# Kernel tuning notes

Measured on AMD Instinct MI355X. Metric: run time of the kernel, lower is better.

## Reference

```python
import jax, jax.numpy as jnp
import numpy as np

B, S, HID = 2, 2048, 2048
H, HKV, D = 8, 4, 256
SW = 1024
SOFTCAP = 50.0
SCALE = D ** -0.5
NEG = -2.3819763e38
ROPE_BASE = 10000.0


def _rope(x, cos, sin):
    # x: [B, S, H, D]; cos/sin: [S, D/2]. Gemma: first half real, second half imag.
    d2 = x.shape[-1] // 2
    x1, x2 = x[..., :d2], x[..., d2:]
    c = cos[None, :, None, :]
    s = sin[None, :, None, :]
    return jnp.concatenate([x1 * c - x2 * s, x1 * s + x2 * c], axis=-1)


def setup_inputs() -> dict:
    key = jax.random.key(0)
    k1, k2, k3, k4, k5, k6 = jax.random.split(key, 6)
    hidden_states = jax.random.normal(k1, (B, S, HID), dtype=jnp.float32)
    # Gemma RoPE freqs_cis -> cos/sin tables [S, D/2]
    inv_freq = 1.0 / (ROPE_BASE ** (np.arange(0, D, 2, dtype=np.float32) / D))
    t = np.arange(S, dtype=np.float32)
    ang = np.outer(t, inv_freq)  # [S, D/2]
    freqs_cos = jnp.asarray(np.cos(ang), dtype=jnp.float32)
    freqs_sin = jnp.asarray(np.sin(ang), dtype=jnp.float32)
    # causal additive mask [1,1,S,S]
    i = jnp.arange(S)
    causal = i[:, None] >= i[None, :]
    mask = jnp.where(causal, 0.0, NEG).astype(jnp.float32)[None, None]
    std = HID ** -0.5
    wq = jax.random.normal(k2, (H * D, HID), dtype=jnp.float32) * std
    wk = jax.random.normal(k3, (HKV * D, HID), dtype=jnp.float32) * std
    wv = jax.random.normal(k4, (HKV * D, HID), dtype=jnp.float32) * std
    wo = jax.random.normal(k5, (HID, H * D), dtype=jnp.float32) * (H * D) ** -0.5
    return {"hidden_states": hidden_states, "freqs_cos": freqs_cos,
            "freqs_sin": freqs_sin, "mask": mask,
            "wq": wq, "wk": wk, "wv": wv, "wo": wo}


def reference(hidden_states, freqs_cos, freqs_sin, mask, wq, wk, wv, wo):
    b, s, _ = hidden_states.shape
    q = (hidden_states @ wq.T).reshape(b, s, H, D)
    k = (hidden_states @ wk.T).reshape(b, s, HKV, D)
    v = (hidden_states @ wv.T).reshape(b, s, HKV, D)
    q = _rope(q, freqs_cos, freqs_sin)
    k = _rope(k, freqs_cos, freqs_sin)
    # GQA: repeat_interleave kv heads to match query heads
    rep = H // HKV
    k = jnp.repeat(k, rep, axis=2)
    v = jnp.repeat(v, rep, axis=2)
    q = q.transpose(0, 2, 1, 3)  # [B,H,S,D]
    k = k.transpose(0, 2, 1, 3)
    v = v.transpose(0, 2, 1, 3)
    # local (sliding window) mask: keep |i-j| <= SW-1, else NEG
    i = jnp.arange(s)
    rel = i[:, None] - i[None, :]
    sliding = jnp.abs(rel) < SW
    mask = jnp.where(sliding[None, None], mask, NEG)
    # scaled scores with tanh logit softcapping
    scores = jnp.einsum('bhqd,bhkd->bhqk', q * SCALE, k)
    scores = jnp.tanh(scores / SOFTCAP) * SOFTCAP
    scores = scores + mask
    probs = jax.nn.softmax(scores.astype(jnp.float32), axis=-1).astype(q.dtype)
    attn_output = jnp.einsum('bhqk,bhkd->bhqd', probs, v)  # [B,H,S,D]
    out = attn_output.transpose(0, 2, 1, 3).reshape(b, s, H * D) @ wo.T
    return out, probs, attn_output
```

## Files before the change

### kernel.cpp

```cpp
#include <hip/hip_runtime.h>
#include <hip/hip_bf16.h>

typedef __bf16 bfx8 __attribute__((ext_vector_type(8)));
typedef float  floatx4 __attribute__((ext_vector_type(4)));

#define B_   2
#define S_   2048
#define HID_ 2048
#define H_   8
#define HKV_ 4
#define D_   256
#define SW_  1024
#define NTOK (B_*S_)

__device__ __forceinline__ bool inputs_are_f32(const void* fc) {
  return *(const unsigned int*)fc == 0x3F800000u;
}

__device__ __forceinline__ bfx8 cvt8(const float* p) {
  floatx4 a = *(const floatx4*)p, b = *(const floatx4*)(p + 4);
  bfx8 r;
#pragma unroll
  for (int i = 0; i < 4; ++i) { r[i] = (__bf16)a[i]; r[i + 4] = (__bf16)b[i]; }
  return r;
}

__device__ __forceinline__ bfx8 ld8(const void* base, size_t eoff, bool f32m) {
  if (f32m) return cvt8((const float*)base + eoff);
  return *(const bfx8*)((const __bf16*)base + eoff);
}

__global__ __launch_bounds__(256)
void cvt_f32_bf16(const void* __restrict__ in, __bf16* __restrict__ out,
                  int n8, const void* __restrict__ fcp)
{
  const bool f32m = inputs_are_f32(fcp);
  int i = blockIdx.x * 256 + threadIdx.x;
  int stride = gridDim.x * 256;
  for (; i < n8; i += stride) {
    if (f32m) ((bfx8*)out)[i] = cvt8((const float*)in + (size_t)i * 8);
    else      ((bfx8*)out)[i] = ((const bfx8*)in)[i];
  }
}

template<int SWZ>
__device__ __forceinline__ void xcd_tile(int& bx, int& by) {
  int gx = gridDim.x;
  int orig = blockIdx.y * gx + blockIdx.x;
  int xcd = orig & 7, loc = orig >> 3;
  if (SWZ == 1) {
    int wpx = gx >> 3;
    if (wpx <= 1) { bx = xcd; by = loc; }
    else { bx = (xcd << 1) + (loc & 1); by = loc >> 1; }
  } else {
    int hpy = gridDim.y >> 3;
    int r = loc / gx;
    by = xcd * hpy + r;
    bx = loc - r * gx;
  }
}

template<int AMODE, int EPI, int DT, int SWZ>
__global__ __launch_bounds__(256)
void gemm_bt(const void* __restrict__ A, const void* __restrict__ Bm,
             void* __restrict__ C, const void* __restrict__ fcp,
             int K, int lda, int ldb, int ldc)
{
  const bool f32m = (DT == 1) ? false : inputs_are_f32(fcp);
  __shared__ __align__(16) __bf16 As[128*40];
  __shared__ __align__(16) __bf16 Bs[128*40];
  const int tid  = threadIdx.x;
  const int lane = tid & 63, wave = tid >> 6;
  int bx, by;
  xcd_tile<SWZ>(bx, by);
  const int m0 = by * 128, n0 = bx * 128;
  const int waveM = (wave >> 1) * 64, waveN = (wave & 1) * 64;
  const int lr = lane & 15, quad = lane >> 4;
  floatx4 acc[4][4] = {};

  for (int k0 = 0; k0 < K; k0 += 32) {
    __syncthreads();
#pragma unroll
    for (int cc = 0; cc < 2; ++cc) {
      int c = tid + cc * 256;
      int row = c >> 2, q = c & 3;
      bfx8 av;
      if (AMODE == 0) {
        av = ld8(A, (size_t)(m0 + row) * lda + (k0 + q * 8), f32m);
      } else {
        int mg = m0 + row, kk = k0 + q * 8;
        size_t aoff = ((size_t)((mg >> 11) * H_ + (kk >> 8)) * S_ + (mg & (S_ - 1))) * D_ + (kk & (D_ - 1));
        av = cvt8((const float*)A + aoff);
      }
      *(bfx8*)(&As[row * 40 + q * 8]) = av;
      *(bfx8*)(&Bs[row * 40 + q * 8]) = ld8(Bm, (size_t)(n0 + row) * ldb + (k0 + q * 8), f32m);
    }
    __syncthreads();
    bfx8 af[4], bfr[4];
#pragma unroll
    for (int im = 0; im < 4; ++im)
      af[im] = *(const bfx8*)(&As[(waveM + im * 16 + lr) * 40 + quad * 8]);
#pragma unroll
    for (int in = 0; in < 4; ++in)
      bfr[in] = *(const bfx8*)(&Bs[(waveN + in * 16 + lr) * 40 + quad * 8]);
#pragma unroll
    for (int im = 0; im < 4; ++im)
#pragma unroll
      for (int in = 0; in < 4; ++in)
        acc[im][in] = __builtin_amdgcn_mfma_f32_16x16x32_bf16(af[im], bfr[in], acc[im][in], 0, 0, 0);
  }

#pragma unroll
  for (int im = 0; im < 4; ++im)
#pragma unroll
    for (int in = 0; in < 4; ++in)
#pragma unroll
      for (int r = 0; r < 4; ++r) {
        int rg = m0 + waveM + im * 16 + quad * 4 + r;
        int cg = n0 + waveN + in * 16 + lr;
        float v = acc[im][in][r];
        if (EPI == 0) ((float*)C)[(size_t)rg * ldc + cg] = v;
        else          ((__bf16*)C)[(size_t)rg * ldc + cg] = (__bf16)v;
      }
}

__global__ __launch_bounds__(256)
void rope_kernel(float* __restrict__ qreg, float* __restrict__ kreg,
                 const void* __restrict__ fc, const void* __restrict__ fs)
{
  const bool f32m = inputs_are_f32(fc);
  int tok = blockIdx.x, t = threadIdx.x;
  int spos = tok & (S_ - 1);
  const float* qrow = qreg + (size_t)tok * 2048;
  const float* krow = kreg + (size_t)tok * 1024;
  float xq1[4], xq2[4], xk1[2], xk2[2];
#pragma unroll
  for (int p = 0; p < 4; ++p) {
    int idx = p * 256 + t, h = idx >> 7, d = idx & 127;
    xq1[p] = qrow[h * 256 + d]; xq2[p] = qrow[h * 256 + d + 128];
  }
#pragma unroll
  for (int p = 0; p < 2; ++p) {
    int idx = p * 256 + t, h = idx >> 7, d = idx & 127;
    xk1[p] = krow[h * 256 + d]; xk2[p] = krow[h * 256 + d + 128];
  }
  __syncthreads();
  __bf16* qo = (__bf16*)qreg + (size_t)tok * 4096;
  __bf16* ko = (__bf16*)kreg + (size_t)tok * 2048;
#pragma unroll
  for (int p = 0; p < 4; ++p) {
    int idx = p * 256 + t, h = idx >> 7, d = idx & 127;
    float c = f32m ? ((const float*)fc)[spos * 128 + d] : (float)((const __bf16*)fc)[spos * 128 + d];
    float s = f32m ? ((const float*)fs)[spos * 128 + d] : (float)((const __bf16*)fs)[spos * 128 + d];
    qo[h * 256 + d]       = (__bf16)((xq1[p] * c - xq2[p] * s) * 0.0625f);
    qo[h * 256 + d + 128] = (__bf16)((xq1[p] * s + xq2[p] * c) * 0.0625f);
  }
#pragma unroll
  for (int p = 0; p < 2; ++p) {
    int idx = p * 256 + t, h = idx >> 7, d = idx & 127;
    float c = f32m ? ((const float*)fc)[spos * 128 + d] : (float)((const __bf16*)fc)[spos * 128 + d];
    float s = f32m ? ((const float*)fs)[spos * 128 + d] : (float)((const __bf16*)fs)[spos * 128 + d];
    ko[h * 256 + d]       = (__bf16)(xk1[p] * c - xk2[p] * s);
    ko[h * 256 + d + 128] = (__bf16)(xk1[p] * s + xk2[p] * c);
  }
}

__global__ __launch_bounds__(256)
void qk_mfma(const __bf16* __restrict__ qr, const __bf16* __restrict__ kr,
             float* __restrict__ probs)
{
  const int bh = blockIdx.z;
  const int b = bh >> 3, h = bh & 7, hkv = h >> 1;
  const int i0 = blockIdx.y * 128;
  const int j0 = i0 - 1024 + blockIdx.x * 128;
  if (j0 + 128 <= 0) return;
  __shared__ __align__(16) __bf16 As[128*40];
  __shared__ __align__(16) __bf16 Bs[128*40];
  const int tid  = threadIdx.x;
  const int lane = tid & 63, wave = tid >> 6;
  const int waveM = (wave >> 1) * 64, waveN = (wave & 1) * 64;
  const int lr = lane & 15, quad = lane >> 4;
  floatx4 acc[4][4] = {};
  const __bf16* qbase = qr + ((size_t)(b * S_) << 12) + h * D_;
  const __bf16* kbase = kr + ((size_t)(b * S_) << 11) + hkv * D_;

  for (int k0 = 0; k0 < D_; k0 += 32) {
    __syncthreads();
#pragma unroll
    for (int cc = 0; cc < 2; ++cc) {
      int c = tid + cc * 256;
      int row = c >> 2, q = c & 3;
      int kk = k0 + q * 8;
      *(bfx8*)(&As[row * 40 + q * 8]) = *(const bfx8*)(qbase + ((size_t)(i0 + row) << 12) + kk);
      int jrow = j0 + row; int jc = jrow < 0 ? 0 : jrow;
      *(bfx8*)(&Bs[row * 40 + q * 8]) = *(const bfx8*)(kbase + ((size_t)jc << 11) + kk);
    }
    __syncthreads();
    bfx8 af[4], bfr[4];
#pragma unroll
    for (int im = 0; im < 4; ++im)
      af[im] = *(const bfx8*)(&As[(waveM + im * 16 + lr) * 40 + quad * 8]);
#pragma unroll
    for (int in = 0; in < 4; ++in)
      bfr[in] = *(const bfx8*)(&Bs[(waveN + in * 16 + lr) * 40 + quad * 8]);
#pragma unroll
    for (int im = 0; im < 4; ++im)
#pragma unroll
      for (int in = 0; in < 4; ++in)
        acc[im][in] = __builtin_amdgcn_mfma_f32_16x16x32_bf16(af[im], bfr[in], acc[im][in], 0, 0, 0);
  }

#pragma unroll
  for (int im = 0; im < 4; ++im)
#pragma unroll
    for (int in = 0; in < 4; ++in)
#pragma unroll
      for (int r = 0; r < 4; ++r) {
        int rg = i0 + waveM + im * 16 + quad * 4 + r;
        int cg = j0 + waveN + in * 16 + lr;
        if (cg >= 0) {
          float v = acc[im][in][r];
          float e = __expf(0.04f * v);
          probs[((size_t)bh * S_ + rg) * 2048 + cg] =
              50.f * (e - 1.f) * __builtin_amdgcn_rcpf(e + 1.f);
        }
      }
}

__global__ __launch_bounds__(256)
void softmax_nat(float* __restrict__ probs)
{
  int i = blockIdx.x, bh = blockIdx.y;
  float* row = probs + ((size_t)bh * S_ + i) * 2048;
  int t = threadIdx.x;
  int jlo = (i >= 1023) ? (i - 1023) : 0;
  __shared__ float red[256];

  float lm = -3.0e38f;
  for (int j = jlo + t; j <= i; j += 256) lm = fmaxf(lm, row[j]);
  red[t] = lm; __syncthreads();
  for (int st = 128; st; st >>= 1) { if (t < st) red[t] = fmaxf(red[t], red[t + st]); __syncthreads(); }
  float mx = red[0]; __syncthreads();

  float ls = 0.f;
  for (int j = jlo + t; j <= i; j += 256) ls += __expf(row[j] - mx);
  red[t] = ls; __syncthreads();
  for (int st = 128; st; st >>= 1) { if (t < st) red[t] += red[t + st]; __syncthreads(); }
  float inv = 1.f / red[0];

  float pv[8];
#pragma unroll
  for (int rep = 0; rep < 8; ++rep) {
    int j = t + rep * 256;
    bool valid = (j >= jlo) && (j <= i);
    pv[rep] = valid ? __expf(row[j] - mx) * inv : 0.f;
  }
  __syncthreads();
#pragma unroll
  for (int rep = 0; rep < 8; ++rep) row[t + rep * 256] = pv[rep];
}

__global__ __launch_bounds__(256)
void transpose_v(const __bf16* __restrict__ vb, __bf16* __restrict__ vt)
{
  __shared__ __align__(16) __bf16 tile[64 * 72];
  int b = blockIdx.z, c0 = blockIdx.y * 64, j0 = blockIdx.x * 64;
  int tid = threadIdx.x;
#pragma unroll
  for (int p = 0; p < 2; ++p) {
    int e = p * 2048 + tid * 8;
    int row = e >> 6, col = e & 63;
    int swz = col ^ (((row >> 3) & 7) * 8);
    *(bfx8*)(&tile[row * 72 + swz]) =
      *(const bfx8*)(vb + ((size_t)(b * S_ + j0 + row) << 10) + c0 + col);
  }
  __syncthreads();
#pragma unroll
  for (int p = 0; p < 2; ++p) {
    int e = p * 2048 + tid * 8;
    int cc = e >> 6, jj = e & 63;
    bfx8 v8;
#pragma unroll
    for (int x = 0; x < 8; ++x) {
      int row = jj + x;
      v8[x] = tile[row * 72 + (cc ^ (((row >> 3) & 7) * 8))];
    }
    *(bfx8*)(vt + ((size_t)(b * 1024 + c0 + cc) << 11) + j0 + jj) = v8;
  }
}

__global__ __launch_bounds__(256)
void pv_mfma(const float* __restrict__ probs, const __bf16* __restrict__ vt,
             float* __restrict__ attn)
{
  const int bh = blockIdx.z;
  const int b = bh >> 3, hkv = (bh & 7) >> 1;
  const int i0 = blockIdx.y * 128;
  const int n0 = blockIdx.x * 128;
  const int kstart = (i0 >= 1024) ? (i0 - 1024) : 0;
  const int kend = i0 + 128;
  __shared__ __align__(16) __bf16 As[128*40];
  __shared__ __align__(16) __bf16 Bs[128*40];
  const int tid  = threadIdx.x;
  const int lane = tid & 63, wave = tid >> 6;
  const int waveM = (wave >> 1) * 64, waveN = (wave & 1) * 64;
  const int lr = lane & 15, quad = lane >> 4;
  floatx4 acc[4][4] = {};
  const float*  abase = probs + ((size_t)bh * S_) * 2048;
  const __bf16* bbase = vt + ((size_t)(b * 1024 + hkv * 256 + n0)) * 2048;

  for (int k0 = kstart; k0 < kend; k0 += 32) {
    __syncthreads();
#pragma unroll
    for (int cc = 0; cc < 2; ++cc) {
      int c = tid + cc * 256;
      int row = c >> 2, q = c & 3;
      int kk = k0 + q * 8;
      *(bfx8*)(&As[row * 40 + q * 8]) = cvt8(abase + (size_t)(i0 + row) * 2048 + kk);
      *(bfx8*)(&Bs[row * 40 + q * 8]) = *(const bfx8*)(bbase + ((size_t)row << 11) + kk);
    }
    __syncthreads();
    bfx8 af[4], bfr[4];
#pragma unroll
    for (int im = 0; im < 4; ++im)
      af[im] = *(const bfx8*)(&As[(waveM + im * 16 + lr) * 40 + quad * 8]);
#pragma unroll
    for (int in = 0; in < 4; ++in)
      bfr[in] = *(const bfx8*)(&Bs[(waveN + in * 16 + lr) * 40 + quad * 8]);
#pragma unroll
    for (int im = 0; im < 4; ++im)
#pragma unroll
      for (int in = 0; in < 4; ++in)
        acc[im][in] = __builtin_amdgcn_mfma_f32_16x16x32_bf16(af[im], bfr[in], acc[im][in], 0, 0, 0);
  }

#pragma unroll
  for (int im = 0; im < 4; ++im)
#pragma unroll
    for (int in = 0; in < 4; ++in)
#pragma unroll
      for (int r = 0; r < 4; ++r) {
        int rg = i0 + waveM + im * 16 + quad * 4 + r;
        int cg = n0 + waveN + in * 16 + lr;
        attn[((size_t)bh * S_ + rg) * D_ + cg] = acc[im][in][r];
      }
}

extern "C" void kernel_launch(void* const* d_in, const int* in_sizes, int n_in,
                              void* d_out, int out_size, void* d_ws, size_t ws_size,
                              hipStream_t stream) {
  (void)in_sizes; (void)n_in; (void)out_size; (void)d_ws; (void)ws_size;
  const void* hidden = d_in[0];
  const void* fc     = d_in[1];
  const void* fs     = d_in[2];
  const void* wq     = d_in[4];
  const void* wk     = d_in[5];
  const void* wv     = d_in[6];
  const void* wo     = d_in[7];

  float* out_r   = (float*)d_out;
  float* probs_r = out_r + (size_t)B_ * S_ * HID_;
  float* attn_r  = probs_r + (size_t)B_ * H_ * S_ * S_;

  float*  qf = attn_r;
  __bf16* qr = (__bf16*)attn_r;
  float*  kf = out_r;
  __bf16* kr = (__bf16*)out_r;
  __bf16* vb = (__bf16*)out_r + 8388608;
  __bf16* vt = (__bf16*)(out_r + 6291456);

  __bf16* hb  = (__bf16*)probs_r;
  __bf16* wqb = hb  + (size_t)NTOK * HID_;
  __bf16* wkb = wqb + (size_t)H_ * D_ * HID_;
  __bf16* wvb = wkb + (size_t)HKV_ * D_ * HID_;

  dim3 blk(256);
  cvt_f32_bf16<<<dim3(1024), blk, 0, stream>>>(hidden, hb,  NTOK * HID_ / 8, fc);
  cvt_f32_bf16<<<dim3(512),  blk, 0, stream>>>(wq, wqb, H_ * D_ * HID_ / 8, fc);
  cvt_f32_bf16<<<dim3(256),  blk, 0, stream>>>(wk, wkb, HKV_ * D_ * HID_ / 8, fc);
  cvt_f32_bf16<<<dim3(256),  blk, 0, stream>>>(wv, wvb, HKV_ * D_ * HID_ / 8, fc);

  gemm_bt<0,0,1,1><<<dim3(16,32), blk, 0, stream>>>(hb, wqb, qf, fc, 2048, 2048, 2048, 2048);
  gemm_bt<0,0,1,1><<<dim3(8,32),  blk, 0, stream>>>(hb, wkb, kf, fc, 2048, 2048, 2048, 1024);
  gemm_bt<0,1,1,1><<<dim3(8,32),  blk, 0, stream>>>(hb, wvb, vb, fc, 2048, 2048, 2048, 1024);
  rope_kernel<<<dim3(NTOK), blk, 0, stream>>>(qf, kf, fc, fs);
  transpose_v<<<dim3(32,16,2), blk, 0, stream>>>(vb, vt);
  qk_mfma<<<dim3(9,16,16), blk, 0, stream>>>(qr, kr, probs_r);
  softmax_nat<<<dim3(2048,16), blk, 0, stream>>>(probs_r);
  pv_mfma<<<dim3(2,16,16), blk, 0, stream>>>(probs_r, vt, attn_r);
  gemm_bt<1,0,0,2><<<dim3(16,32), blk, 0, stream>>>(attn_r, wo, out_r, fc, 2048, 2048, 2048, 2048);
}
```

Baseline: 859.8 us.

## Fuse QK scores with softmax via two-pass recompute and widen PV tile

Replaces the separate QK score kernel and row softmax kernel with one kernel. It keeps a 64-row Q tile in LDS and runs over the sliding-window K tiles twice: the first pass builds row sums and the second recomputes scores and writes normalized probabilities. It uses a fixed exponent offset, which is safe because the tanh softcap bounds scores to ±50. The block also zero-fills the masked regions, so the full probs matrix is written once instead of written, read and rewritten. The PV kernel is widened to cover all 256 head columns per block, so each probs tile is loaded and converted once rather than twice. The cost is doubled QK MFMA work, lower occupancy from 64KB of LDS, and more accumulator registers in PV.

New measurement: 837.3 us. 2.6% less time.

```diff
diff --git a/kernel.cpp b/kernel.cpp
--- a/kernel.cpp
+++ b/kernel.cpp
@@ -166,98 +166,91 @@
 }
 
 __global__ __launch_bounds__(256)
-void qk_mfma(const __bf16* __restrict__ qr, const __bf16* __restrict__ kr,
-             float* __restrict__ probs)
-{
-  const int bh = blockIdx.z;
-  const int b = bh >> 3, h = bh & 7, hkv = h >> 1;
-  const int i0 = blockIdx.y * 128;
-  const int j0 = i0 - 1024 + blockIdx.x * 128;
-  if (j0 + 128 <= 0) return;
-  __shared__ __align__(16) __bf16 As[128*40];
-  __shared__ __align__(16) __bf16 Bs[128*40];
-  const int tid  = threadIdx.x;
-  const int lane = tid & 63, wave = tid >> 6;
-  const int waveM = (wave >> 1) * 64, waveN = (wave & 1) * 64;
+void qk_fused(const __bf16* __restrict__ qr, const __bf16* __restrict__ kr,
+              float* __restrict__ probs)
+{
+  const int bh = blockIdx.y, b = bh >> 3, h = bh & 7, hkv = h >> 1;
+  const int i0 = blockIdx.x * 64;
+  __shared__ __align__(16) __bf16 Qs[64*256];
+  __shared__ __align__(16) __bf16 Ks[64*256];
+  const int tid = threadIdx.x, lane = tid & 63, wave = tid >> 6;
   const int lr = lane & 15, quad = lane >> 4;
-  floatx4 acc[4][4] = {};
-  const __bf16* qbase = qr + ((size_t)(b * S_) << 12) + h * D_;
+  const int sx = lr & 7;
+  const __bf16* qbase = qr + ((size_t)(b * S_ + i0) << 12) + h * D_;
   const __bf16* kbase = kr + ((size_t)(b * S_) << 11) + hkv * D_;
 
-  for (int k0 = 0; k0 < D_; k0 += 32) {
-    __syncthreads();
-#pragma unroll
-    for (int cc = 0; cc < 2; ++cc) {
-      int c = tid + cc * 256;
-      int row = c >> 2, q = c & 3;
-      int kk = k0 + q * 8;
-      *(bfx8*)(&As[row * 40 + q * 8]) = *(const bfx8*)(qbase + ((size_t)(i0 + row) << 12) + kk);
-      int jrow = j0 + row; int jc = jrow < 0 ? 0 : jrow;
-      *(bfx8*)(&Bs[row * 40 + q * 8]) = *(const bfx8*)(kbase + ((size_t)jc << 11) + kk);
-    }
-    __syncthreads();
-    bfx8 af[4], bfr[4];
-#pragma unroll
-    for (int im = 0; im < 4; ++im)
-      af[im] = *(const bfx8*)(&As[(waveM + im * 16 + lr) * 40 + quad * 8]);
-#pragma unroll
-    for (int in = 0; in < 4; ++in)
-      bfr[in] = *(const bfx8*)(&Bs[(waveN + in * 16 + lr) * 40 + quad * 8]);
-#pragma unroll
-    for (int im = 0; im < 4; ++im)
+#pragma unroll
+  for (int p = 0; p < 8; ++p) {
+    int c = tid + p * 256;
+    int row = c >> 5, ch = c & 31;
+    *(bfx8*)(&Qs[row * 256 + (ch ^ (row & 7)) * 8]) =
+        *(const bfx8*)(qbase + ((size_t)row << 12) + ch * 8);
+  }
+
+  const int jt0 = (i0 >= 1024) ? 0 : (16 - (i0 >> 6));
+  const int myrow = wave * 16 + quad * 4;
+  float psum[4] = {0.f, 0.f, 0.f, 0.f};
+  float inv[4];
+
+  for (int pass = 0; pass < 2; ++pass) {
+    for (int jt = jt0; jt <= 16; ++jt) {
+      int j0 = i0 - 1024 + jt * 64;
+      __syncthreads();
+#pragma unroll
+      for (int p = 0; p < 8; ++p) {
+        int c = tid + p * 256;
+        int row = c >> 5, ch = c & 31;
+        *(bfx8*)(&Ks[row * 256 + (ch ^ (row & 7)) * 8]) =
+            *(const bfx8*)(kbase + ((size_t)(j0 + row) << 11) + ch * 8);
+      }
+      __syncthreads();
+      floatx4 acc[4] = {};
+#pragma unroll
+      for (int ks = 0; ks < 8; ++ks) {
+        bfx8 af = *(const bfx8*)(&Qs[(wave * 16 + lr) * 256 + ((ks * 4 + quad) ^ sx) * 8]);
+#pragma unroll
+        for (int in = 0; in < 4; ++in) {
+          bfx8 bf = *(const bfx8*)(&Ks[(in * 16 + lr) * 256 + ((ks * 4 + quad) ^ sx) * 8]);
+          acc[in] = __builtin_amdgcn_mfma_f32_16x16x32_bf16(af, bf, acc[in], 0, 0, 0);
+        }
+      }
 #pragma unroll
       for (int in = 0; in < 4; ++in)
-        acc[im][in] = __builtin_amdgcn_mfma_f32_16x16x32_bf16(af[im], bfr[in], acc[im][in], 0, 0, 0);
-  }
-
-#pragma unroll
-  for (int im = 0; im < 4; ++im)
-#pragma unroll
-    for (int in = 0; in < 4; ++in)
+#pragma unroll
+        for (int r = 0; r < 4; ++r) {
+          int rg = i0 + myrow + r;
+          int cg = j0 + in * 16 + lr;
+          bool valid = (cg <= rg) && (rg - cg < SW_);
+          float v = acc[in][r];
+          float e = __expf(0.04f * v);
+          float sc = 50.f * (e - 1.f) * __builtin_amdgcn_rcpf(e + 1.f);
+          float pp = valid ? __expf(sc - 30.f) : 0.f;
+          if (pass == 0) psum[r] += pp;
+          else probs[((size_t)bh * S_ + rg) * 2048 + cg] = pp * inv[r];
+        }
+    }
+    if (pass == 0) {
 #pragma unroll
       for (int r = 0; r < 4; ++r) {
-        int rg = i0 + waveM + im * 16 + quad * 4 + r;
-        int cg = j0 + waveN + in * 16 + lr;
-        if (cg >= 0) {
-          float v = acc[im][in][r];
-          float e = __expf(0.04f * v);
-          probs[((size_t)bh * S_ + rg) * 2048 + cg] =
-              50.f * (e - 1.f) * __builtin_amdgcn_rcpf(e + 1.f);
-        }
-      }
-}
-
-__global__ __launch_bounds__(256)
-void softmax_nat(float* __restrict__ probs)
-{
-  int i = blockIdx.x, bh = blockIdx.y;
-  float* row = probs + ((size_t)bh * S_ + i) * 2048;
-  int t = threadIdx.x;
-  int jlo = (i >= 1023) ? (i - 1023) : 0;
-  __shared__ float red[256];
-
-  float lm = -3.0e38f;
-  for (int j = jlo + t; j <= i; j += 256) lm = fmaxf(lm, row[j]);
-  red[t] = lm; __syncthreads();
-  for (int st = 128; st; st >>= 1) { if (t < st) red[t] = fmaxf(red[t], red[t + st]); __syncthreads(); }
-  float mx = red[0]; __syncthreads();
-
-  float ls = 0.f;
-  for (int j = jlo + t; j <= i; j += 256) ls += __expf(row[j] - mx);
-  red[t] = ls; __syncthreads();
-  for (int st = 128; st; st >>= 1) { if (t < st) red[t] += red[t + st]; __syncthreads(); }
-  float inv = 1.f / red[0];
-
-  float pv[8];
-#pragma unroll
-  for (int rep = 0; rep < 8; ++rep) {
-    int j = t + rep * 256;
-    bool valid = (j >= jlo) && (j <= i);
-    pv[rep] = valid ? __expf(row[j] - mx) * inv : 0.f;
-  }
-  __syncthreads();
-#pragma unroll
-  for (int rep = 0; rep < 8; ++rep) row[t + rep * 256] = pv[rep];
+        float s = psum[r];
+        s += __shfl_xor(s, 1); s += __shfl_xor(s, 2);
+        s += __shfl_xor(s, 4); s += __shfl_xor(s, 8);
+        inv[r] = 1.f / s;
+      }
+    }
+  }
+
+  {
+    int L = (i0 >= 1024) ? (i0 - 1024) : 0;
+    int R = i0 + 64;
+    float* pb = probs + ((size_t)bh * S_ + i0) * 2048;
+    int nL4 = L >> 2, nR4 = (2048 - R) >> 2;
+    for (int r = 0; r < 64; ++r) {
+      float* rowp = pb + (size_t)r * 2048;
+      for (int c = tid; c < nL4; c += 256) ((floatx4*)rowp)[c] = (floatx4){0.f, 0.f, 0.f, 0.f};
+      for (int c = tid; c < nR4; c += 256) *(floatx4*)(rowp + R + c * 4) = (floatx4){0.f, 0.f, 0.f, 0.f};
+    }
+  }
 }
 
 __global__ __launch_bounds__(256)
@@ -290,58 +283,60 @@
 }
 
 __global__ __launch_bounds__(256)
-void pv_mfma(const float* __restrict__ probs, const __bf16* __restrict__ vt,
+void pv_wide(const float* __restrict__ probs, const __bf16* __restrict__ vt,
              float* __restrict__ attn)
 {
-  const int bh = blockIdx.z;
+  const int bh = blockIdx.y;
   const int b = bh >> 3, hkv = (bh & 7) >> 1;
-  const int i0 = blockIdx.y * 128;
-  const int n0 = blockIdx.x * 128;
+  const int i0 = blockIdx.x * 128;
   const int kstart = (i0 >= 1024) ? (i0 - 1024) : 0;
   const int kend = i0 + 128;
   __shared__ __align__(16) __bf16 As[128*40];
-  __shared__ __align__(16) __bf16 Bs[128*40];
+  __shared__ __align__(16) __bf16 Bs[256*40];
   const int tid  = threadIdx.x;
   const int lane = tid & 63, wave = tid >> 6;
-  const int waveM = (wave >> 1) * 64, waveN = (wave & 1) * 64;
+  const int waveM = (wave >> 1) * 64, waveN = (wave & 1) * 128;
   const int lr = lane & 15, quad = lane >> 4;
-  floatx4 acc[4][4] = {};
+  floatx4 acc[4][8] = {};
   const float*  abase = probs + ((size_t)bh * S_) * 2048;
-  const __bf16* bbase = vt + ((size_t)(b * 1024 + hkv * 256 + n0)) * 2048;
+  const __bf16* bbase = vt + ((size_t)(b * 1024 + hkv * 256)) * 2048;
 
   for (int k0 = kstart; k0 < kend; k0 += 32) {
     __syncthreads();
 #pragma unroll
-    for (int cc = 0; cc < 2; ++cc) {
-      int c = tid + cc * 256;
-      int row = c >> 2, q = c & 3;
-      int kk = k0 + q * 8;
-      *(bfx8*)(&As[row * 40 + q * 8]) = cvt8(abase + (size_t)(i0 + row) * 2048 + kk);
-      *(bfx8*)(&Bs[row * 40 + q * 8]) = *(const bfx8*)(bbase + ((size_t)row << 11) + kk);
+    for (int p = 0; p < 6; ++p) {
+      int c = tid + p * 256;
+      if (p < 2) {
+        int row = c >> 2, q = c & 3, kk = k0 + q * 8;
+        *(bfx8*)(&As[row * 40 + q * 8]) = cvt8(abase + (size_t)(i0 + row) * 2048 + kk);
+      } else {
+        int c2 = c - 512;
+        int row = c2 >> 2, q = c2 & 3, kk = k0 + q * 8;
+        *(bfx8*)(&Bs[row * 40 + q * 8]) = *(const bfx8*)(bbase + ((size_t)row << 11) + kk);
+      }
     }
     __syncthreads();
-    bfx8 af[4], bfr[4];
+    bfx8 af[4];
 #pragma unroll
     for (int im = 0; im < 4; ++im)
       af[im] = *(const bfx8*)(&As[(waveM + im * 16 + lr) * 40 + quad * 8]);
 #pragma unroll
-    for (int in = 0; in < 4; ++in)
-      bfr[in] = *(const bfx8*)(&Bs[(waveN + in * 16 + lr) * 40 + quad * 8]);
-#pragma unroll
-    for (int im = 0; im < 4; ++im)
-#pragma unroll
-      for (int in = 0; in < 4; ++in)
-        acc[im][in] = __builtin_amdgcn_mfma_f32_16x16x32_bf16(af[im], bfr[in], acc[im][in], 0, 0, 0);
+    for (int in = 0; in < 8; ++in) {
+      bfx8 bf = *(const bfx8*)(&Bs[(waveN + in * 16 + lr) * 40 + quad * 8]);
+#pragma unroll
+      for (int im = 0; im < 4; ++im)
+        acc[im][in] = __builtin_amdgcn_mfma_f32_16x16x32_bf16(af[im], bf, acc[im][in], 0, 0, 0);
+    }
   }
 
 #pragma unroll
   for (int im = 0; im < 4; ++im)
 #pragma unroll
-    for (int in = 0; in < 4; ++in)
+    for (int in = 0; in < 8; ++in)
 #pragma unroll
       for (int r = 0; r < 4; ++r) {
         int rg = i0 + waveM + im * 16 + quad * 4 + r;
-        int cg = n0 + waveN + in * 16 + lr;
+        int cg = waveN + in * 16 + lr;
         attn[((size_t)bh * S_ + rg) * D_ + cg] = acc[im][in][r];
       }
 }
@@ -385,8 +380,7 @@
   gemm_bt<0,1,1,1><<<dim3(8,32),  blk, 0, stream>>>(hb, wvb, vb, fc, 2048, 2048, 2048, 1024);
   rope_kernel<<<dim3(NTOK), blk, 0, stream>>>(qf, kf, fc, fs);
   transpose_v<<<dim3(32,16,2), blk, 0, stream>>>(vb, vt);
-  qk_mfma<<<dim3(9,16,16), blk, 0, stream>>>(qr, kr, probs_r);
-  softmax_nat<<<dim3(2048,16), blk, 0, stream>>>(probs_r);
-  pv_mfma<<<dim3(2,16,16), blk, 0, stream>>>(probs_r, vt, attn_r);
+  qk_fused<<<dim3(32,16), blk, 0, stream>>>(qr, kr, probs_r);
+  pv_wide<<<dim3(16,16), blk, 0, stream>>>(probs_r, vt, attn_r);
   gemm_bt<1,0,0,2><<<dim3(16,32), blk, 0, stream>>>(attn_r, wo, out_r, fc, 2048, 2048, 2048, 2048);
 }
```
